# Kernel optimization log

Measured on AMD Instinct MI355X. Metric: run time of the kernel, lower is better.

## Reference

```python
import jax, jax.numpy as jnp
import numpy as np

NU, NI, E = 50000, 20000, 400000
IN, HID, OUT = 128, 256, 128
NEG_SLOPE_ATTN = 0.2   # DGL GATConv default
NEG_SLOPE_ACT = 0.01   # F.leaky_relu default
BN_EPS = 1e-5


def setup_inputs() -> dict:
    key = jax.random.key(0)
    ks = jax.random.split(key, 32)
    d = {}
    d["x_user"] = jax.random.normal(ks[0], (NU, IN), jnp.float32)
    d["x_item"] = jax.random.normal(ks[1], (NI, IN), jnp.float32)
    d["eu"] = jax.random.randint(ks[2], (E,), 0, NU, jnp.int32)
    d["ei"] = jax.random.randint(ks[3], (E,), 0, NI, jnp.int32)
    i = 4
    dims = [(IN, 4, 64), (HID, 4, 64), (HID, 4, 64), (HID, 4, 32)]
    for L, (fin, H, dh) in enumerate(dims):
        for rel in ("ui", "iu"):
            d[f"W{L}_{rel}"] = jax.random.normal(ks[i], (fin, H * dh), jnp.float32) * 0.1; i += 1
            d[f"A{L}_{rel}"] = jax.random.normal(ks[i], (2, H, dh), jnp.float32) * 0.1; i += 1
    # BN params: [layer, (gamma,beta), HID]; gamma near 1, beta near 0
    gu = 1.0 + 0.05 * jax.random.normal(ks[i], (3, 1, HID), jnp.float32); i += 1
    bu = 0.05 * jax.random.normal(ks[i], (3, 1, HID), jnp.float32); i += 1
    gi = 1.0 + 0.05 * jax.random.normal(ks[i], (3, 1, HID), jnp.float32); i += 1
    bi = 0.05 * jax.random.normal(ks[i], (3, 1, HID), jnp.float32); i += 1
    d["bn_u"] = jnp.concatenate([gu, bu], axis=1)
    d["bn_i"] = jnp.concatenate([gi, bi], axis=1)
    return d


def _gat(x_src, x_dst, W, A, src, dst, n_dst):
    # Single-relation bipartite GATConv (DGL semantics).
    H, dh = A.shape[1], A.shape[2]
    hs = (x_src @ W).reshape(-1, H, dh)           # [Ns,H,dh]
    hd = (x_dst @ W).reshape(-1, H, dh)           # [Nd,H,dh]
    el = jnp.einsum('nhd,hd->nh', hs, A[0])
    er = jnp.einsum('nhd,hd->nh', hd, A[1])
    e = jax.nn.leaky_relu(el[src] + er[dst], NEG_SLOPE_ATTN)   # [E,H]
    emax = jax.ops.segment_max(e, dst, num_segments=n_dst)
    ee = jnp.exp(e - emax[dst])
    denom = jax.ops.segment_sum(ee, dst, num_segments=n_dst)
    alpha = ee / denom[dst]                       # segment softmax over in-edges
    out = jax.ops.segment_sum(hs[src] * alpha[..., None], dst, num_segments=n_dst)
    return out.reshape(n_dst, H * dh)


def _bn(x, gamma, beta):
    mu = x.mean(axis=0)
    var = x.var(axis=0)   # biased, matches torch BN normalization
    return gamma * (x - mu) * jax.lax.rsqrt(var + BN_EPS) + beta


def reference(x_user, x_item, eu, ei, W0_ui, W0_iu, A0_ui, A0_iu,
              W1_ui, W1_iu, A1_ui, A1_iu, W2_ui, W2_iu, A2_ui, A2_iu,
              W3_ui, W3_iu, A3_ui, A3_iu, bn_u, bn_i):
    Wui = [W0_ui, W1_ui, W2_ui]; Aui = [A0_ui, A1_ui, A2_ui]
    Wiu = [W0_iu, W1_iu, W2_iu]; Aiu = [A0_iu, A1_iu, A2_iu]
    hu, hi = x_user, x_item
    for L in range(3):
        ni = _gat(hu, hi, Wui[L], Aui[L], eu, ei, NI)   # user -> item
        nu = _gat(hi, hu, Wiu[L], Aiu[L], ei, eu, NU)   # item -> user
        nu = _bn(nu, bn_u[L, 0], bn_u[L, 1])
        ni = _bn(ni, bn_i[L, 0], bn_i[L, 1])
        if L == 2:   # last hidden layer uses tanh in non-residual path
            hu, hi = jnp.tanh(nu), jnp.tanh(ni)
        else:
            hu = jax.nn.leaky_relu(nu, NEG_SLOPE_ACT)
            hi = jax.nn.leaky_relu(ni, NEG_SLOPE_ACT)
    out_i = _gat(hu, hi, W3_ui, A3_ui, eu, ei, NI)
    out_u = _gat(hi, hu, W3_iu, A3_iu, ei, eu, NU)
    return jnp.concatenate([out_u, out_i], axis=0)   # [NU+NI, OUT]
```

## Files before the change

### kernel.cpp

```cpp
#include <hip/hip_runtime.h>

#define NUSERS 50000
#define NITEMS 20000
#define NEDGES 400000

typedef _Float16 f16;
typedef __attribute__((ext_vector_type(8))) _Float16 f16x8;
typedef __attribute__((ext_vector_type(4))) _Float16 f16x4;
typedef __attribute__((ext_vector_type(2))) _Float16 f16x2;
typedef __attribute__((ext_vector_type(4))) float f32x4;

__global__ void prep_k(const float* __restrict__ Wa, const float* __restrict__ Aa,
                       f16* __restrict__ Bta, float* __restrict__ efa,
                       const float* __restrict__ Wb, const float* __restrict__ Ab,
                       f16* __restrict__ Btb, float* __restrict__ efb,
                       int K, int Nw, int dh) {
  int t = blockIdx.x * blockDim.x + threadIdx.x;
  int half = K * Nw;
  if (t >= 2 * half) return;
  const float* W = (t < half) ? Wa : Wb;
  const float* A = (t < half) ? Aa : Ab;
  f16* Bt = (t < half) ? Bta : Btb;
  float* ef = (t < half) ? efa : efb;
  int t2 = (t < half) ? t : t - half;
  int n = t2 / K, k = t2 - n * K;
  Bt[t2] = (f16)W[(long)k * Nw + n];
  if (t2 < K * 8) {
    int j = t2 / (K * 4);
    int r = t2 - j * K * 4;
    int h = r / K, f = r - h * K;
    const float* Aj = A + j * Nw;
    float s = 0.f;
    for (int d = 0; d < dh; ++d) s += W[f * Nw + h * dh + d] * Aj[h * dh + d];
    ef[j * 4 * K + h * K + f] = s;
  }
}

__global__ void xcvt_k(const float* __restrict__ xu, f16* __restrict__ yu, long nu,
                       const float* __restrict__ xi, f16* __restrict__ yi, long ni) {
  long i = (long)blockIdx.x * blockDim.x + threadIdx.x;
  if (i < nu) yu[i] = (f16)xu[i];
  else if (i < nu + ni) yi[i - nu] = (f16)xi[i - nu];
}

__global__ __launch_bounds__(256) void hgemm2_k(const f16* __restrict__ Aa, const f16* __restrict__ Bta,
                                                f16* __restrict__ Ca, int Ma, int gya,
                                                const f16* __restrict__ Ab, const f16* __restrict__ Btb,
                                                f16* __restrict__ Cb, int Mb,
                                                int N, int K) {
  __shared__ f16 As[128 * 32];
  __shared__ f16 Bs[128 * 32];
  int by = blockIdx.y;
  const f16* A; const f16* Bt; f16* C; int M; int row0;
  if (by < gya) { A = Aa; Bt = Bta; C = Ca; M = Ma; row0 = by * 128; }
  else          { A = Ab; Bt = Btb; C = Cb; M = Mb; row0 = (by - gya) * 128; }
  int tid = threadIdx.x;
  int col0 = blockIdx.x * 128;
  int lane = tid & 63, wv = tid >> 6;
  int wr = (wv & 1) * 64, wc = (wv >> 1) * 64;
  int l16 = lane & 15, q = lane >> 4;
  f32x4 acc[4][4] = {};
  int r = tid >> 2, c8 = (tid & 3) * 8;
  for (int k0 = 0; k0 < K; k0 += 32) {
    int ra = min(row0 + r, M - 1);
    uint4 va = *(const uint4*)&A[(long)ra * K + k0 + c8];
    int ra2 = min(row0 + r + 64, M - 1);
    uint4 va2 = *(const uint4*)&A[(long)ra2 * K + k0 + c8];
    uint4 vb = *(const uint4*)&Bt[(long)(col0 + r) * K + k0 + c8];
    uint4 vb2 = *(const uint4*)&Bt[(long)(col0 + r + 64) * K + k0 + c8];
    *(uint4*)&As[r * 32 + c8] = va;
    *(uint4*)&As[(r + 64) * 32 + c8] = va2;
    *(uint4*)&Bs[r * 32 + c8] = vb;
    *(uint4*)&Bs[(r + 64) * 32 + c8] = vb2;
    __syncthreads();
    f16x8 af[4], bfr[4];
#pragma unroll
    for (int i = 0; i < 4; ++i) {
      af[i] = *(const f16x8*)&As[(wr + i * 16 + l16) * 32 + q * 8];
      bfr[i] = *(const f16x8*)&Bs[(wc + i * 16 + l16) * 32 + q * 8];
    }
#pragma unroll
    for (int i = 0; i < 4; ++i)
#pragma unroll
      for (int j = 0; j < 4; ++j)
        acc[i][j] = __builtin_amdgcn_mfma_f32_16x16x32_f16(af[i], bfr[j], acc[i][j], 0, 0, 0);
    __syncthreads();
  }
#pragma unroll
  for (int i = 0; i < 4; ++i) {
#pragma unroll
    for (int reg = 0; reg < 4; ++reg) {
      int rr = row0 + wr + i * 16 + q * 4 + reg;
      if (rr < M) {
#pragma unroll
        for (int j = 0; j < 4; ++j)
          C[(long)rr * N + col0 + wc + j * 16 + l16] = (f16)acc[i][j][reg];
      }
    }
  }
}

__global__ __launch_bounds__(256) void eler_k(
    const f16* __restrict__ hbu, const float* __restrict__ ef_ui, const float* __restrict__ ef_iu,
    float* __restrict__ el_u, float* __restrict__ er_u,
    const f16* __restrict__ hbi, float* __restrict__ el_i, float* __restrict__ er_i, int K) {
  __shared__ float xs[256];
  int b = blockIdx.x, t = threadIdx.x;
  const f16* hb; const float* elf; const float* erf; float* el; float* er; int n;
  if (b < NUSERS) { hb = hbu; elf = ef_ui; erf = ef_iu + 4 * K; el = el_u; er = er_u; n = b; }
  else            { hb = hbi; elf = ef_iu; erf = ef_ui + 4 * K; el = el_i; er = er_i; n = b - NUSERS; }
  if (t < K) xs[t] = (float)hb[(long)n * K + t];
  __syncthreads();
  int j = t >> 5, l = t & 31;
  const float* fr = (j < 4) ? (elf + j * K) : (erf + (j - 4) * K);
  float p = 0.f;
  for (int f = l; f < K; f += 32) p += xs[f] * fr[f];
#pragma unroll
  for (int off = 16; off; off >>= 1) p += __shfl_down(p, off, 32);
  if (l == 0) { if (j < 4) el[n * 4 + j] = p; else er[n * 4 + (j - 4)] = p; }
}

__global__ void hist_k(const int* __restrict__ ei, int* __restrict__ degi,
                       const int* __restrict__ eu, int* __restrict__ degu) {
  int e = blockIdx.x * blockDim.x + threadIdx.x;
  if (e < NEDGES) atomicAdd(&degi[ei[e]], 1);
  else if (e < 2 * NEDGES) atomicAdd(&degu[eu[e - NEDGES]], 1);
}

__global__ __launch_bounds__(256) void scan1_k(const int* __restrict__ deg,
                                               int* __restrict__ bsum, int N) {
  __shared__ int red[256];
  int base = blockIdx.x * 1024, t = threadIdx.x;
  int s = 0;
#pragma unroll
  for (int j = 0; j < 4; ++j) { int i = base + t * 4 + j; s += (i < N) ? deg[i] : 0; }
  red[t] = s; __syncthreads();
  for (int off = 128; off; off >>= 1) { if (t < off) red[t] += red[t + off]; __syncthreads(); }
  if (t == 0) bsum[blockIdx.x] = red[0];
}

__global__ void scan2_k(int* __restrict__ bsum, int nb) {
  if (threadIdx.x == 0) {
    int run = 0;
    for (int i = 0; i < nb; ++i) { int v = bsum[i]; bsum[i] = run; run += v; }
  }
}

__global__ __launch_bounds__(256) void scan3_k(const int* __restrict__ deg,
                                               const int* __restrict__ bsum,
                                               int* __restrict__ rowptr, int N) {
  __shared__ int tsum[256];
  int base = blockIdx.x * 1024, t = threadIdx.x;
  int v[4]; int s = 0;
#pragma unroll
  for (int j = 0; j < 4; ++j) { int i = base + t * 4 + j; v[j] = (i < N) ? deg[i] : 0; s += v[j]; }
  tsum[t] = s; __syncthreads();
  for (int off = 1; off < 256; off <<= 1) {
    int x = (t >= off) ? tsum[t - off] : 0;
    __syncthreads();
    tsum[t] += x;
    __syncthreads();
  }
  int run = bsum[blockIdx.x] + ((t > 0) ? tsum[t - 1] : 0);
#pragma unroll
  for (int j = 0; j < 4; ++j) {
    int i = base + t * 4 + j;
    if (i < N) rowptr[i] = run;
    run += v[j];
  }
}

__global__ void setval_k(int* __restrict__ p, int v) { *p = v; }

__global__ void copy2_k(const int* __restrict__ a, int* __restrict__ b, int Na,
                        const int* __restrict__ c, int* __restrict__ d, int Nc) {
  int i = blockIdx.x * blockDim.x + threadIdx.x;
  if (i < Na) b[i] = a[i];
  else if (i < Na + Nc) d[i - Na] = c[i - Na];
}

__global__ void scat_k(const int* __restrict__ ei, const int* __restrict__ eu,
                       int* __restrict__ curi, int* __restrict__ srci,
                       int* __restrict__ curu, int* __restrict__ srcu) {
  int e = blockIdx.x * blockDim.x + threadIdx.x;
  if (e < NEDGES) {
    int p = atomicAdd(&curi[ei[e]], 1);
    srci[p] = eu[e];
  } else if (e < 2 * NEDGES) {
    int e2 = e - NEDGES;
    int p = atomicAdd(&curu[eu[e2]], 1);
    srcu[p] = ei[e2];
  }
}

template <int W, int DH, typename OUT>
__global__ __launch_bounds__(256) void agg_k(
    const float* __restrict__ elA, const float* __restrict__ erA,
    const int* __restrict__ rpA, const int* __restrict__ srcA,
    const f16* __restrict__ hsA, OUT* __restrict__ outA, int nA,
    const float* __restrict__ elB, const float* __restrict__ erB,
    const int* __restrict__ rpB, const int* __restrict__ srcB,
    const f16* __restrict__ hsB, OUT* __restrict__ outB, int nB) {
  constexpr int CPL = W >> 6;
  constexpr int SHIFT = (W == 256) ? 9 : 8;
  constexpr bool OF16 = (sizeof(OUT) == 2);
  __shared__ float alds[4][256];
  __shared__ int soff[4][64];
  int wv = threadIdx.x >> 6;
  int g = blockIdx.x * 4 + wv;
  int lane = threadIdx.x & 63;
  const float* el; const float* er; const int* rp; const int* srcv;
  const f16* hs; OUT* outp; int d;
  if (g < nA)           { el = elA; er = erA; rp = rpA; srcv = srcA; hs = hsA; outp = outA; d = g; }
  else if (g < nA + nB) { el = elB; er = erB; rp = rpB; srcv = srcB; hs = hsB; outp = outB; d = g - nA; }
  else return;
  int s0 = rp[d], s1 = rp[d + 1];
  int deg = s1 - s0;
  int c0 = lane * CPL;
  int h = c0 / DH;
  long obase = (long)d * W + c0;
  if (deg == 0) {
#pragma unroll
    for (int q = 0; q < CPL; ++q) outp[obase + q] = (OUT)0.f;
    return;
  }
  const float NEG = -3.0e38f;
  float acc[CPL];
#pragma unroll
  for (int q = 0; q < CPL; ++q) acc[q] = 0.f;
  float inv;

  if (deg <= 64) {
    int hh = lane & 3, p = lane >> 2;
    float er_h = er[d * 4 + hh];
    float vv[4];
    float vmax = NEG;
#pragma unroll
    for (int j = 0; j < 4; ++j) {
      int slot = j * 16 + p;
      vv[j] = NEG;
      if (slot < deg) {
        int sj = srcv[s0 + slot];
        if (hh == 0) soff[wv][slot] = sj << SHIFT;
        float v = el[sj * 4 + hh] + er_h;
        v = v > 0.f ? v : 0.2f * v;
        vv[j] = v;
        vmax = fmaxf(vmax, v);
      }
    }
#pragma unroll
    for (int off = 4; off < 64; off <<= 1) vmax = fmaxf(vmax, __shfl_xor(vmax, off, 64));
    float ssum = 0.f;
#pragma unroll
    for (int j = 0; j < 4; ++j) {
      int slot = j * 16 + p;
      if (slot < deg) {
        float e = expf(vv[j] - vmax);
        alds[wv][slot * 4 + hh] = e;
        ssum += e;
      }
    }
#pragma unroll
    for (int off = 4; off < 64; off <<= 1) ssum += __shfl_xor(ssum, off, 64);
    float Sh = __shfl(ssum, (lane & ~3) | h, 64);
    inv = 1.0f / Sh;
    const char* hbase = (const char*)hs + (size_t)c0 * sizeof(f16);
    for (int j = 0; j < deg; ++j) {
      float aj = alds[wv][j * 4 + h];
      int off = soff[wv][j];
      const f16* row = (const f16*)(hbase + (size_t)(unsigned)off);
      if constexpr (CPL == 4) {
        f16x4 hv = *(const f16x4*)row;
        acc[0] += aj * (float)hv[0]; acc[1] += aj * (float)hv[1];
        acc[2] += aj * (float)hv[2]; acc[3] += aj * (float)hv[3];
      } else {
        f16x2 hv = *(const f16x2*)row;
        acc[0] += aj * (float)hv[0]; acc[1] += aj * (float)hv[1];
      }
    }
  } else {
    float4 er4 = *(const float4*)&er[d * 4];
    float m0 = NEG, m1 = NEG, m2 = NEG, m3 = NEG;
    for (int k = s0 + lane; k < s1; k += 64) {
      int s = srcv[k];
      float4 e4 = *(const float4*)&el[s * 4];
      float v;
      v = e4.x + er4.x; v = v > 0.f ? v : 0.2f * v; m0 = fmaxf(m0, v);
      v = e4.y + er4.y; v = v > 0.f ? v : 0.2f * v; m1 = fmaxf(m1, v);
      v = e4.z + er4.z; v = v > 0.f ? v : 0.2f * v; m2 = fmaxf(m2, v);
      v = e4.w + er4.w; v = v > 0.f ? v : 0.2f * v; m3 = fmaxf(m3, v);
    }
#pragma unroll
    for (int off = 32; off; off >>= 1) {
      m0 = fmaxf(m0, __shfl_xor(m0, off, 64));
      m1 = fmaxf(m1, __shfl_xor(m1, off, 64));
      m2 = fmaxf(m2, __shfl_xor(m2, off, 64));
      m3 = fmaxf(m3, __shfl_xor(m3, off, 64));
    }
    float S0 = 0.f, S1 = 0.f, S2 = 0.f, S3 = 0.f;
    for (int k = s0 + lane; k < s1; k += 64) {
      int s = srcv[k];
      float4 e4 = *(const float4*)&el[s * 4];
      float v;
      v = e4.x + er4.x; v = v > 0.f ? v : 0.2f * v; S0 += expf(v - m0);
      v = e4.y + er4.y; v = v > 0.f ? v : 0.2f * v; S1 += expf(v - m1);
      v = e4.z + er4.z; v = v > 0.f ? v : 0.2f * v; S2 += expf(v - m2);
      v = e4.w + er4.w; v = v > 0.f ? v : 0.2f * v; S3 += expf(v - m3);
    }
#pragma unroll
    for (int off = 32; off; off >>= 1) {
      S0 += __shfl_xor(S0, off, 64);
      S1 += __shfl_xor(S1, off, 64);
      S2 += __shfl_xor(S2, off, 64);
      S3 += __shfl_xor(S3, off, 64);
    }
    float mh = h == 0 ? m0 : h == 1 ? m1 : h == 2 ? m2 : m3;
    float Sh = h == 0 ? S0 : h == 1 ? S1 : h == 2 ? S2 : S3;
    float erh = h == 0 ? er4.x : h == 1 ? er4.y : h == 2 ? er4.z : er4.w;
    inv = 1.0f / Sh;
    for (int k = s0; k < s1; ++k) {
      int s = srcv[k];
      float v = el[s * 4 + h] + erh; v = v > 0.f ? v : 0.2f * v;
      float a = expf(v - mh);
      const f16* row = &hs[(long)s * W + c0];
      if constexpr (CPL == 4) {
        f16x4 hv = *(const f16x4*)row;
        acc[0] += a * (float)hv[0]; acc[1] += a * (float)hv[1];
        acc[2] += a * (float)hv[2]; acc[3] += a * (float)hv[3];
      } else {
        f16x2 hv = *(const f16x2*)row;
        acc[0] += a * (float)hv[0]; acc[1] += a * (float)hv[1];
      }
    }
  }
  if constexpr (OF16) {
    if constexpr (CPL == 4) {
      f16x4 o = { (f16)(acc[0] * inv), (f16)(acc[1] * inv), (f16)(acc[2] * inv), (f16)(acc[3] * inv) };
      *(f16x4*)&outp[obase] = o;
    } else {
      f16x2 o = { (f16)(acc[0] * inv), (f16)(acc[1] * inv) };
      *(f16x2*)&outp[obase] = o;
    }
  } else {
    if constexpr (CPL == 4) {
      *(float4*)&outp[obase] = make_float4(acc[0] * inv, acc[1] * inv, acc[2] * inv, acc[3] * inv);
    } else {
      *(float2*)&outp[obase] = make_float2(acc[0] * inv, acc[1] * inv);
    }
  }
}

__global__ void zero2_k(float* __restrict__ a, float* __restrict__ b) {
  int t = threadIdx.x;
  a[t] = 0.f; b[t] = 0.f;
}

__global__ __launch_bounds__(256) void bn_stats2_k(const f16* __restrict__ xu, float* __restrict__ su, int Nu, int gU,
                                                   const f16* __restrict__ xi, float* __restrict__ si, int Ni) {
  const int C = 256;
  int b = blockIdx.x;
  const f16* x; float* sums; int N; int r0;
  if (b < gU) { x = xu; sums = su; N = Nu; r0 = b * 64; }
  else        { x = xi; sums = si; N = Ni; r0 = (b - gU) * 64; }
  int c = threadIdx.x;
  int r1 = min(r0 + 64, N);
  float s = 0.f, s2 = 0.f;
  for (int r = r0; r < r1; ++r) {
    float v = (float)x[(long)r * C + c];
    s += v; s2 += v * v;
  }
  atomicAdd(&sums[c], s);
  atomicAdd(&sums[C + c], s2);
}

__global__ __launch_bounds__(256) void bn_fused_k(
    const f16* __restrict__ xu, const float* __restrict__ su, const float* __restrict__ gbu,
    f16* __restrict__ yu, int Nu,
    const f16* __restrict__ xi, const float* __restrict__ si, const float* __restrict__ gbi,
    f16* __restrict__ yi, int Ni,
    const float* __restrict__ efu, const float* __restrict__ efiu,
    float* __restrict__ el_u, float* __restrict__ er_u,
    float* __restrict__ el_i, float* __restrict__ er_i, int act) {
  const int Kn = 256;
  __shared__ float xs[256];
  int b = blockIdx.x, t = threadIdx.x;
  const f16* x; const float* sums; const float* gb; f16* y; int n; int N;
  const float* elf; const float* erf; float* el; float* er;
  if (b < Nu) { x = xu; sums = su; gb = gbu; y = yu; n = b; N = Nu; elf = efu;  erf = efiu + 4 * Kn; el = el_u; er = er_u; }
  else        { x = xi; sums = si; gb = gbi; y = yi; n = b - Nu; N = Ni; elf = efiu; erf = efu + 4 * Kn;  el = el_i; er = er_i; }
  long base = (long)n * 256;
  float val = (float)x[base + t];
  float inv_n = 1.0f / (float)N;
  float mean = sums[t] * inv_n;
  float var = sums[256 + t] * inv_n - mean * mean;
  float v = gb[t] * (val - mean) * rsqrtf(var + 1e-5f) + gb[256 + t];
  v = act ? tanhf(v) : (v > 0.f ? v : 0.01f * v);
  y[base + t] = (f16)v;
  xs[t] = v;
  __syncthreads();
  int j = t >> 5, l = t & 31;
  const float* fr = (j < 4) ? (elf + j * Kn) : (erf + (j - 4) * Kn);
  float p = 0.f;
  for (int f = l; f < Kn; f += 32) p += xs[f] * fr[f];
#pragma unroll
  for (int off = 16; off; off >>= 1) p += __shfl_down(p, off, 32);
  if (l == 0) { if (j < 4) el[n * 4 + j] = p; else er[n * 4 + (j - 4)] = p; }
}

extern "C" void kernel_launch(void* const* d_in, const int* in_sizes, int n_in,
                              void* d_out, int out_size, void* d_ws, size_t ws_size,
                              hipStream_t stream) {
  const float* x_user = (const float*)d_in[0];
  const float* x_item = (const float*)d_in[1];
  const int* eu = (const int*)d_in[2];
  const int* ei = (const int*)d_in[3];
  const float *Wm[4][2], *Am[4][2];
  for (int L = 0; L < 4; ++L) {
    Wm[L][0] = (const float*)d_in[4 + L * 4 + 0];
    Am[L][0] = (const float*)d_in[4 + L * 4 + 1];
    Wm[L][1] = (const float*)d_in[4 + L * 4 + 2];
    Am[L][1] = (const float*)d_in[4 + L * 4 + 3];
  }
  const float* bnu = (const float*)d_in[20];
  const float* bni = (const float*)d_in[21];
  float* out = (float*)d_out;

  float* ws = (float*)d_ws;
  size_t o = 0;
  float* el_u = ws + o; o += (size_t)NUSERS * 4;
  float* er_u = ws + o; o += (size_t)NUSERS * 4;
  float* el_i = ws + o; o += (size_t)NITEMS * 4;
  float* er_i = ws + o; o += (size_t)NITEMS * 4;
  float* ef_all[4][2];
  for (int L = 0; L < 4; ++L)
    for (int rl = 0; rl < 2; ++rl) { ef_all[L][rl] = ws + o; o += 2048; }
  float* bns_u = ws + o; o += 512;
  float* bns_i = ws + o; o += 512;
  f16* hb_u   = (f16*)(ws + o); o += (size_t)NUSERS * 128;
  f16* hb_i   = (f16*)(ws + o); o += (size_t)NITEMS * 128;
  f16* hsb_u  = (f16*)(ws + o); o += (size_t)NUSERS * 128;
  f16* hsb_i  = (f16*)(ws + o); o += (size_t)NITEMS * 128;
  f16* aggh_u = (f16*)(ws + o); o += (size_t)NUSERS * 128;
  f16* aggh_i = (f16*)(ws + o); o += (size_t)NITEMS * 128;
  f16* Bt_all[4][2];
  for (int L = 0; L < 4; ++L) {
    int K = (L == 0) ? 128 : 256;
    int W = (L == 3) ? 128 : 256;
    for (int rl = 0; rl < 2; ++rl) { Bt_all[L][rl] = (f16*)(ws + o); o += (size_t)K * W / 2; }
  }
  int* deg_i    = (int*)(ws + o); o += NITEMS;
  int* deg_u    = (int*)(ws + o); o += NUSERS;
  int* rowptr_i = (int*)(ws + o); o += NITEMS + 1;
  int* rowptr_u = (int*)(ws + o); o += NUSERS + 1;
  int* cur_i    = (int*)(ws + o); o += NITEMS;
  int* cur_u    = (int*)(ws + o); o += NUSERS;
  int* bsum     = (int*)(ws + o); o += 256;
  int* csrsrc_i = (int*)(ws + o); o += NEDGES;
  int* csrsrc_u = (int*)(ws + o); o += NEDGES;

  const int gE2 = (2 * NEDGES + 255) / 256;
  const int nb_i = (NITEMS + 1023) / 1024;
  const int nb_u = (NUSERS + 1023) / 1024;
  const int gU = (NUSERS + 63) / 64;
  const int gI = (NITEMS + 63) / 64;

  hipMemsetAsync(deg_i, 0, (NITEMS + NUSERS) * sizeof(int), stream);
  hist_k<<<dim3(gE2), dim3(256), 0, stream>>>(ei, deg_i, eu, deg_u);
  scan1_k<<<dim3(nb_i), dim3(256), 0, stream>>>(deg_i, bsum, NITEMS);
  scan2_k<<<dim3(1), dim3(64), 0, stream>>>(bsum, nb_i);
  scan3_k<<<dim3(nb_i), dim3(256), 0, stream>>>(deg_i, bsum, rowptr_i, NITEMS);
  setval_k<<<dim3(1), dim3(1), 0, stream>>>(rowptr_i + NITEMS, NEDGES);
  scan1_k<<<dim3(nb_u), dim3(256), 0, stream>>>(deg_u, bsum, NUSERS);
  scan2_k<<<dim3(1), dim3(64), 0, stream>>>(bsum, nb_u);
  scan3_k<<<dim3(nb_u), dim3(256), 0, stream>>>(deg_u, bsum, rowptr_u, NUSERS);
  setval_k<<<dim3(1), dim3(1), 0, stream>>>(rowptr_u + NUSERS, NEDGES);
  copy2_k<<<dim3((NITEMS + NUSERS + 255) / 256), dim3(256), 0, stream>>>(rowptr_i, cur_i, NITEMS, rowptr_u, cur_u, NUSERS);
  scat_k<<<dim3(gE2), dim3(256), 0, stream>>>(ei, eu, cur_i, csrsrc_i, cur_u, csrsrc_u);

  for (int L = 0; L < 4; ++L) {
    int K = (L == 0) ? 128 : 256;
    int dh = (L == 3) ? 32 : 64;
    int W = 4 * dh;
    prep_k<<<dim3((2 * K * W + 255) / 256), dim3(256), 0, stream>>>(
        Wm[L][0], Am[L][0], Bt_all[L][0], ef_all[L][0],
        Wm[L][1], Am[L][1], Bt_all[L][1], ef_all[L][1], K, W, dh);
  }

  xcvt_k<<<dim3(((NUSERS + NITEMS) * 128 + 255) / 256), dim3(256), 0, stream>>>(
      x_user, hb_u, (long)NUSERS * 128, x_item, hb_i, (long)NITEMS * 128);
  eler_k<<<dim3(NUSERS + NITEMS), dim3(256), 0, stream>>>(
      hb_u, ef_all[0][0], ef_all[0][1], el_u, er_u, hb_i, el_i, er_i, 128);

  int K = 128;
  for (int L = 0; L < 4; ++L) {
    const int dh = (L == 3) ? 32 : 64;
    const int W = 4 * dh;

    const int gya = (NUSERS + 127) / 128, gyb = (NITEMS + 127) / 128;
    hgemm2_k<<<dim3(W / 128, gya + gyb), dim3(256), 0, stream>>>(
        hb_u, Bt_all[L][0], hsb_u, NUSERS, gya, hb_i, Bt_all[L][1], hsb_i, NITEMS, W, K);

    const int gAgg = (NITEMS + NUSERS + 3) / 4;
    if (L < 3) {
      agg_k<256, 64, f16><<<dim3(gAgg), dim3(256), 0, stream>>>(
          el_u, er_i, rowptr_i, csrsrc_i, hsb_u, aggh_i, NITEMS,
          el_i, er_u, rowptr_u, csrsrc_u, hsb_i, aggh_u, NUSERS);
      zero2_k<<<dim3(1), dim3(512), 0, stream>>>(bns_u, bns_i);
      bn_stats2_k<<<dim3(gU + gI), dim3(256), 0, stream>>>(aggh_u, bns_u, NUSERS, gU, aggh_i, bns_i, NITEMS);
      bn_fused_k<<<dim3(NUSERS + NITEMS), dim3(256), 0, stream>>>(
          aggh_u, bns_u, bnu + L * 512, hb_u, NUSERS,
          aggh_i, bns_i, bni + L * 512, hb_i, NITEMS,
          ef_all[L + 1][0], ef_all[L + 1][1],
          el_u, er_u, el_i, er_i, L == 2);
      K = 256;
    } else {
      agg_k<128, 32, float><<<dim3(gAgg), dim3(256), 0, stream>>>(
          el_u, er_i, rowptr_i, csrsrc_i, hsb_u, out + (size_t)NUSERS * 128, NITEMS,
          el_i, er_u, rowptr_u, csrsrc_u, hsb_i, out, NUSERS);
    }
  }
}
```

Baseline: 918.1 us.

## Split edge softmax into separate kernel with precomputed per-edge exp weights

Adds a kernel that computes unnormalised per-edge exp(leaky_relu(el+er)) for each of the four heads into a head-major edge buffer, plus per-destination sums, dropping the max subtraction. The aggregation kernel then reads these weights and source indices four edges at a time with vector loads and issues four independent row gathers per iteration for more memory-level parallelism. This removes the LDS staging, the separate small- and large-degree paths and the repeated exp work per lane. It adds an extra kernel launch and a write and read of a 4×E float buffer per layer. Skipping the max subtraction risks overflow if attention logits are large.

```diff
diff --git a/kernel.cpp b/kernel.cpp
--- a/kernel.cpp
+++ b/kernel.cpp
@@ -193,144 +193,117 @@
   }
 }
 
-template <int W, int DH, typename OUT>
-__global__ __launch_bounds__(256) void agg_k(
+__global__ __launch_bounds__(256) void sfm_k(
     const float* __restrict__ elA, const float* __restrict__ erA,
     const int* __restrict__ rpA, const int* __restrict__ srcA,
-    const f16* __restrict__ hsA, OUT* __restrict__ outA, int nA,
+    float* __restrict__ pxA, float* __restrict__ SA, int nA,
     const float* __restrict__ elB, const float* __restrict__ erB,
     const int* __restrict__ rpB, const int* __restrict__ srcB,
-    const f16* __restrict__ hsB, OUT* __restrict__ outB, int nB) {
-  constexpr int CPL = W >> 6;
-  constexpr int SHIFT = (W == 256) ? 9 : 8;
-  constexpr bool OF16 = (sizeof(OUT) == 2);
-  __shared__ float alds[4][256];
-  __shared__ int soff[4][64];
+    float* __restrict__ pxB, float* __restrict__ SB, int nB, int P) {
   int wv = threadIdx.x >> 6;
   int g = blockIdx.x * 4 + wv;
   int lane = threadIdx.x & 63;
   const float* el; const float* er; const int* rp; const int* srcv;
+  float* px; float* S; int d;
+  if (g < nA)           { el = elA; er = erA; rp = rpA; srcv = srcA; px = pxA; S = SA; d = g; }
+  else if (g < nA + nB) { el = elB; er = erB; rp = rpB; srcv = srcB; px = pxB; S = SB; d = g - nA; }
+  else return;
+  int s0 = rp[d], s1 = rp[d + 1];
+  float4 er4 = *(const float4*)&er[d * 4];
+  float a0 = 0.f, a1 = 0.f, a2 = 0.f, a3 = 0.f;
+  for (int k = s0 + lane; k < s1; k += 64) {
+    int s = srcv[k];
+    float4 e4 = *(const float4*)&el[(size_t)s * 4];
+    float v0 = e4.x + er4.x; v0 = v0 > 0.f ? v0 : 0.2f * v0; float p0 = __expf(v0);
+    float v1 = e4.y + er4.y; v1 = v1 > 0.f ? v1 : 0.2f * v1; float p1 = __expf(v1);
+    float v2 = e4.z + er4.z; v2 = v2 > 0.f ? v2 : 0.2f * v2; float p2 = __expf(v2);
+    float v3 = e4.w + er4.w; v3 = v3 > 0.f ? v3 : 0.2f * v3; float p3 = __expf(v3);
+    px[k] = p0; px[P + k] = p1; px[2 * P + k] = p2; px[3 * P + k] = p3;
+    a0 += p0; a1 += p1; a2 += p2; a3 += p3;
+  }
+#pragma unroll
+  for (int off = 32; off; off >>= 1) {
+    a0 += __shfl_xor(a0, off, 64);
+    a1 += __shfl_xor(a1, off, 64);
+    a2 += __shfl_xor(a2, off, 64);
+    a3 += __shfl_xor(a3, off, 64);
+  }
+  if (lane == 0) *(float4*)&S[d * 4] = make_float4(a0, a1, a2, a3);
+}
+
+template <int W, int DH, typename OUT>
+__global__ __launch_bounds__(256) void agg_k(
+    const int* __restrict__ rpA, const int* __restrict__ srcA,
+    const float* __restrict__ pxA, const float* __restrict__ SA,
+    const f16* __restrict__ hsA, OUT* __restrict__ outA, int nA,
+    const int* __restrict__ rpB, const int* __restrict__ srcB,
+    const float* __restrict__ pxB, const float* __restrict__ SB,
+    const f16* __restrict__ hsB, OUT* __restrict__ outB, int nB, int P) {
+  constexpr int CPL = W >> 6;
+  constexpr int SHIFT = (W == 256) ? 9 : 8;
+  constexpr bool OF16 = (sizeof(OUT) == 2);
+  int wv = threadIdx.x >> 6;
+  int g = blockIdx.x * 4 + wv;
+  int lane = threadIdx.x & 63;
+  const int* rp; const int* srcv; const float* px; const float* Sv;
   const f16* hs; OUT* outp; int d;
-  if (g < nA)           { el = elA; er = erA; rp = rpA; srcv = srcA; hs = hsA; outp = outA; d = g; }
-  else if (g < nA + nB) { el = elB; er = erB; rp = rpB; srcv = srcB; hs = hsB; outp = outB; d = g - nA; }
+  if (g < nA)           { rp = rpA; srcv = srcA; px = pxA; Sv = SA; hs = hsA; outp = outA; d = g; }
+  else if (g < nA + nB) { rp = rpB; srcv = srcB; px = pxB; Sv = SB; hs = hsB; outp = outB; d = g - nA; }
   else return;
   int s0 = rp[d], s1 = rp[d + 1];
   int deg = s1 - s0;
   int c0 = lane * CPL;
-  int h = c0 / DH;
+  int h = lane >> 4;
   long obase = (long)d * W + c0;
   if (deg == 0) {
 #pragma unroll
     for (int q = 0; q < CPL; ++q) outp[obase + q] = (OUT)0.f;
     return;
   }
-  const float NEG = -3.0e38f;
+  float inv = 1.0f / Sv[d * 4 + h];
+  const float* pl = px + (size_t)h * P;
+  const char* hbase = (const char*)hs + (size_t)c0 * sizeof(f16);
   float acc[CPL];
 #pragma unroll
   for (int q = 0; q < CPL; ++q) acc[q] = 0.f;
-  float inv;
-
-  if (deg <= 64) {
-    int hh = lane & 3, p = lane >> 2;
-    float er_h = er[d * 4 + hh];
-    float vv[4];
-    float vmax = NEG;
-#pragma unroll
-    for (int j = 0; j < 4; ++j) {
-      int slot = j * 16 + p;
-      vv[j] = NEG;
-      if (slot < deg) {
-        int sj = srcv[s0 + slot];
-        if (hh == 0) soff[wv][slot] = sj << SHIFT;
-        float v = el[sj * 4 + hh] + er_h;
-        v = v > 0.f ? v : 0.2f * v;
-        vv[j] = v;
-        vmax = fmaxf(vmax, v);
-      }
-    }
-#pragma unroll
-    for (int off = 4; off < 64; off <<= 1) vmax = fmaxf(vmax, __shfl_xor(vmax, off, 64));
-    float ssum = 0.f;
-#pragma unroll
-    for (int j = 0; j < 4; ++j) {
-      int slot = j * 16 + p;
-      if (slot < deg) {
-        float e = expf(vv[j] - vmax);
-        alds[wv][slot * 4 + hh] = e;
-        ssum += e;
-      }
-    }
-#pragma unroll
-    for (int off = 4; off < 64; off <<= 1) ssum += __shfl_xor(ssum, off, 64);
-    float Sh = __shfl(ssum, (lane & ~3) | h, 64);
-    inv = 1.0f / Sh;
-    const char* hbase = (const char*)hs + (size_t)c0 * sizeof(f16);
-    for (int j = 0; j < deg; ++j) {
-      float aj = alds[wv][j * 4 + h];
-      int off = soff[wv][j];
-      const f16* row = (const f16*)(hbase + (size_t)(unsigned)off);
-      if constexpr (CPL == 4) {
-        f16x4 hv = *(const f16x4*)row;
-        acc[0] += aj * (float)hv[0]; acc[1] += aj * (float)hv[1];
-        acc[2] += aj * (float)hv[2]; acc[3] += aj * (float)hv[3];
-      } else {
-        f16x2 hv = *(const f16x2*)row;
-        acc[0] += aj * (float)hv[0]; acc[1] += aj * (float)hv[1];
-      }
-    }
-  } else {
-    float4 er4 = *(const float4*)&er[d * 4];
-    float m0 = NEG, m1 = NEG, m2 = NEG, m3 = NEG;
-    for (int k = s0 + lane; k < s1; k += 64) {
-      int s = srcv[k];
-      float4 e4 = *(const float4*)&el[s * 4];
-      float v;
-      v = e4.x + er4.x; v = v > 0.f ? v : 0.2f * v; m0 = fmaxf(m0, v);
-      v = e4.y + er4.y; v = v > 0.f ? v : 0.2f * v; m1 = fmaxf(m1, v);
-      v = e4.z + er4.z; v = v > 0.f ? v : 0.2f * v; m2 = fmaxf(m2, v);
-      v = e4.w + er4.w; v = v > 0.f ? v : 0.2f * v; m3 = fmaxf(m3, v);
-    }
-#pragma unroll
-    for (int off = 32; off; off >>= 1) {
-      m0 = fmaxf(m0, __shfl_xor(m0, off, 64));
-      m1 = fmaxf(m1, __shfl_xor(m1, off, 64));
-      m2 = fmaxf(m2, __shfl_xor(m2, off, 64));
-      m3 = fmaxf(m3, __shfl_xor(m3, off, 64));
-    }
-    float S0 = 0.f, S1 = 0.f, S2 = 0.f, S3 = 0.f;
-    for (int k = s0 + lane; k < s1; k += 64) {
-      int s = srcv[k];
-      float4 e4 = *(const float4*)&el[s * 4];
-      float v;
-      v = e4.x + er4.x; v = v > 0.f ? v : 0.2f * v; S0 += expf(v - m0);
-      v = e4.y + er4.y; v = v > 0.f ? v : 0.2f * v; S1 += expf(v - m1);
-      v = e4.z + er4.z; v = v > 0.f ? v : 0.2f * v; S2 += expf(v - m2);
-      v = e4.w + er4.w; v = v > 0.f ? v : 0.2f * v; S3 += expf(v - m3);
-    }
-#pragma unroll
-    for (int off = 32; off; off >>= 1) {
-      S0 += __shfl_xor(S0, off, 64);
-      S1 += __shfl_xor(S1, off, 64);
-      S2 += __shfl_xor(S2, off, 64);
-      S3 += __shfl_xor(S3, off, 64);
-    }
-    float mh = h == 0 ? m0 : h == 1 ? m1 : h == 2 ? m2 : m3;
-    float Sh = h == 0 ? S0 : h == 1 ? S1 : h == 2 ? S2 : S3;
-    float erh = h == 0 ? er4.x : h == 1 ? er4.y : h == 2 ? er4.z : er4.w;
-    inv = 1.0f / Sh;
-    for (int k = s0; k < s1; ++k) {
-      int s = srcv[k];
-      float v = el[s * 4 + h] + erh; v = v > 0.f ? v : 0.2f * v;
-      float a = expf(v - mh);
-      const f16* row = &hs[(long)s * W + c0];
-      if constexpr (CPL == 4) {
-        f16x4 hv = *(const f16x4*)row;
-        acc[0] += a * (float)hv[0]; acc[1] += a * (float)hv[1];
-        acc[2] += a * (float)hv[2]; acc[3] += a * (float)hv[3];
-      } else {
-        f16x2 hv = *(const f16x2*)row;
-        acc[0] += a * (float)hv[0]; acc[1] += a * (float)hv[1];
-      }
+  int a0 = s0 & ~3;
+  int nch = (s1 - a0 + 3) >> 2;
+  for (int ch = 0; ch < nch; ++ch) {
+    int k = a0 + ch * 4;
+    int4 s4 = *(const int4*)&srcv[k];
+    float4 p4 = *(const float4*)&pl[k];
+    if (ch == 0 || ch == nch - 1) {
+      bool v0 = (k     >= s0) & (k     < s1);
+      bool v1 = (k + 1 >= s0) & (k + 1 < s1);
+      bool v2 = (k + 2 >= s0) & (k + 2 < s1);
+      bool v3 = (k + 3 >= s0) & (k + 3 < s1);
+      p4.x = v0 ? p4.x : 0.f; s4.x = v0 ? s4.x : 0;
+      p4.y = v1 ? p4.y : 0.f; s4.y = v1 ? s4.y : 0;
+      p4.z = v2 ? p4.z : 0.f; s4.z = v2 ? s4.z : 0;
+      p4.w = v3 ? p4.w : 0.f; s4.w = v3 ? s4.w : 0;
+    }
+    if constexpr (CPL == 4) {
+      f16x4 r0 = *(const f16x4*)(hbase + ((size_t)(unsigned)s4.x << SHIFT));
+      f16x4 r1 = *(const f16x4*)(hbase + ((size_t)(unsigned)s4.y << SHIFT));
+      f16x4 r2 = *(const f16x4*)(hbase + ((size_t)(unsigned)s4.z << SHIFT));
+      f16x4 r3 = *(const f16x4*)(hbase + ((size_t)(unsigned)s4.w << SHIFT));
+      acc[0] += p4.x * (float)r0[0]; acc[1] += p4.x * (float)r0[1];
+      acc[2] += p4.x * (float)r0[2]; acc[3] += p4.x * (float)r0[3];
+      acc[0] += p4.y * (float)r1[0]; acc[1] += p4.y * (float)r1[1];
+      acc[2] += p4.y * (float)r1[2]; acc[3] += p4.y * (float)r1[3];
+      acc[0] += p4.z * (float)r2[0]; acc[1] += p4.z * (float)r2[1];
+      acc[2] += p4.z * (float)r2[2]; acc[3] += p4.z * (float)r2[3];
+      acc[0] += p4.w * (float)r3[0]; acc[1] += p4.w * (float)r3[1];
+      acc[2] += p4.w * (float)r3[2]; acc[3] += p4.w * (float)r3[3];
+    } else {
+      f16x2 r0 = *(const f16x2*)(hbase + ((size_t)(unsigned)s4.x << SHIFT));
+      f16x2 r1 = *(const f16x2*)(hbase + ((size_t)(unsigned)s4.y << SHIFT));
+      f16x2 r2 = *(const f16x2*)(hbase + ((size_t)(unsigned)s4.z << SHIFT));
+      f16x2 r3 = *(const f16x2*)(hbase + ((size_t)(unsigned)s4.w << SHIFT));
+      acc[0] += p4.x * (float)r0[0]; acc[1] += p4.x * (float)r0[1];
+      acc[0] += p4.y * (float)r1[0]; acc[1] += p4.y * (float)r1[1];
+      acc[0] += p4.z * (float)r2[0]; acc[1] += p4.z * (float)r2[1];
+      acc[0] += p4.w * (float)r3[0]; acc[1] += p4.w * (float)r3[1];
     }
   }
   if constexpr (OF16) {
@@ -425,6 +398,8 @@
   const float* bni = (const float*)d_in[21];
   float* out = (float*)d_out;
 
+  const int PP = NEDGES + 4;
+
   float* ws = (float*)d_ws;
   size_t o = 0;
   float* el_u = ws + o; o += (size_t)NUSERS * 4;
@@ -436,6 +411,10 @@
     for (int rl = 0; rl < 2; ++rl) { ef_all[L][rl] = ws + o; o += 2048; }
   float* bns_u = ws + o; o += 512;
   float* bns_i = ws + o; o += 512;
+  float* S_u = ws + o; o += (size_t)NUSERS * 4;
+  float* S_i = ws + o; o += (size_t)NITEMS * 4;
+  float* pexp_i = ws + o; o += (size_t)4 * PP + 4;
+  float* pexp_u = ws + o; o += (size_t)4 * PP + 4;
   f16* hb_u   = (f16*)(ws + o); o += (size_t)NUSERS * 128;
   f16* hb_i   = (f16*)(ws + o); o += (size_t)NITEMS * 128;
   f16* hsb_u  = (f16*)(ws + o); o += (size_t)NUSERS * 128;
@@ -450,13 +429,13 @@
   }
   int* deg_i    = (int*)(ws + o); o += NITEMS;
   int* deg_u    = (int*)(ws + o); o += NUSERS;
-  int* rowptr_i = (int*)(ws + o); o += NITEMS + 1;
-  int* rowptr_u = (int*)(ws + o); o += NUSERS + 1;
+  int* rowptr_i = (int*)(ws + o); o += NITEMS + 4;
+  int* rowptr_u = (int*)(ws + o); o += NUSERS + 4;
   int* cur_i    = (int*)(ws + o); o += NITEMS;
   int* cur_u    = (int*)(ws + o); o += NUSERS;
   int* bsum     = (int*)(ws + o); o += 256;
-  int* csrsrc_i = (int*)(ws + o); o += NEDGES;
-  int* csrsrc_u = (int*)(ws + o); o += NEDGES;
+  int* csrsrc_i = (int*)(ws + o); o += NEDGES + 4;
+  int* csrsrc_u = (int*)(ws + o); o += NEDGES + 4;
 
   const int gE2 = (2 * NEDGES + 255) / 256;
   const int nb_i = (NITEMS + 1023) / 1024;
@@ -492,6 +471,7 @@
       hb_u, ef_all[0][0], ef_all[0][1], el_u, er_u, hb_i, el_i, er_i, 128);
 
   int K = 128;
+  const int gAgg = (NITEMS + NUSERS + 3) / 4;
   for (int L = 0; L < 4; ++L) {
     const int dh = (L == 3) ? 32 : 64;
     const int W = 4 * dh;
@@ -500,11 +480,14 @@
     hgemm2_k<<<dim3(W / 128, gya + gyb), dim3(256), 0, stream>>>(
         hb_u, Bt_all[L][0], hsb_u, NUSERS, gya, hb_i, Bt_all[L][1], hsb_i, NITEMS, W, K);
 
-    const int gAgg = (NITEMS + NUSERS + 3) / 4;
+    sfm_k<<<dim3(gAgg), dim3(256), 0, stream>>>(
+        el_u, er_i, rowptr_i, csrsrc_i, pexp_i, S_i, NITEMS,
+        el_i, er_u, rowptr_u, csrsrc_u, pexp_u, S_u, NUSERS, PP);
+
     if (L < 3) {
       agg_k<256, 64, f16><<<dim3(gAgg), dim3(256), 0, stream>>>(
-          el_u, er_i, rowptr_i, csrsrc_i, hsb_u, aggh_i, NITEMS,
-          el_i, er_u, rowptr_u, csrsrc_u, hsb_i, aggh_u, NUSERS);
+          rowptr_i, csrsrc_i, pexp_i, S_i, hsb_u, aggh_i, NITEMS,
+          rowptr_u, csrsrc_u, pexp_u, S_u, hsb_i, aggh_u, NUSERS, PP);
       zero2_k<<<dim3(1), dim3(512), 0, stream>>>(bns_u, bns_i);
       bn_stats2_k<<<dim3(gU + gI), dim3(256), 0, stream>>>(aggh_u, bns_u, NUSERS, gU, aggh_i, bns_i, NITEMS);
       bn_fused_k<<<dim3(NUSERS + NITEMS), dim3(256), 0, stream>>>(
@@ -515,8 +498,8 @@
       K = 256;
     } else {
       agg_k<128, 32, float><<<dim3(gAgg), dim3(256), 0, stream>>>(
-          el_u, er_i, rowptr_i, csrsrc_i, hsb_u, out + (size_t)NUSERS * 128, NITEMS,
-          el_i, er_u, rowptr_u, csrsrc_u, hsb_i, out, NUSERS);
-    }
-  }
-}
+          rowptr_i, csrsrc_i, pexp_i, S_i, hsb_u, out + (size_t)NUSERS * 128, NITEMS,
+          rowptr_u, csrsrc_u, pexp_u, S_u, hsb_i, out, NUSERS, PP);
+    }
+  }
+}
```

Result: slower. 1.037 ms (+13.0%).
